# Kernel tuning notes

Hardware: AMD Instinct MI355X
Metric: run time of the kernel (lower is better)

## Reference

```python
import jax, jax.numpy as jnp
import numpy as np

LR = 0.01
DECAY = 0.9


def setup_inputs() -> dict:
    key = jax.random.key(0)
    ks = jax.random.split(key, 8)
    B, D_IN, H, N_FLUX, N_MET, N_IN, N_REF = 32768, 128, 1024, 512, 256, 128, 64
    return {
        "input": jax.random.normal(ks[0], (B, D_IN), jnp.float32),
        "Vref": jax.random.normal(ks[1], (B, N_REF), jnp.float32),
        "Vin": jax.random.normal(ks[2], (B, N_IN), jnp.float32),
        "W1": jax.random.normal(ks[3], (D_IN, H), jnp.float32) * 0.02,
        "b1": jnp.zeros((H,), jnp.float32),
        "W2": jax.random.normal(ks[4], (H, N_FLUX), jnp.float32) * 0.02,
        "b2": jnp.zeros((N_FLUX,), jnp.float32),
        "S": jax.random.normal(ks[5], (N_MET, N_FLUX), jnp.float32) * 0.1,
        "Pin": jax.random.normal(ks[6], (N_IN, N_FLUX), jnp.float32) * 0.1,
        "n_iteration": 30,
    }


def reference(input, Vref, Vin, W1, b1, W2, b2, S, Pin, n_iteration):
    # MLP head: Linear -> ReLU -> (Dropout inactive at eval) -> Linear
    V0 = jnp.maximum(input @ W1 + b1, 0.0) @ W2 + b2  # [B, n_flux]
    n_met = S.shape[0]
    n_in = Pin.shape[0]
    n_flux = V0.shape[1]

    def step(carry, _):
        V, diff = carry
        # dL2/dV = 2/n_met * (V S^T) S
        dV2 = (V @ S.T) @ S * (2.0 / n_met)
        # dL3/dV = 2/n_in * relu(V Pin^T - Vin) Pin  (indicator*relu == relu)
        relu_vin = jnp.maximum(V @ Pin.T - Vin, 0.0)
        dV3 = relu_vin @ Pin * (2.0 / n_in)
        # dL4/dV = -2/n_flux * relu(-V) = 2/n_flux * min(V, 0)
        dV4 = jnp.minimum(V, 0.0) * (2.0 / n_flux)
        dV = dV2 + dV3 + dV4
        diff_new = DECAY * diff - LR * dV
        return (V + diff_new, diff_new), None

    (V, _), _ = jax.lax.scan(step, (V0, jnp.zeros_like(V0)), None, length=n_iteration)
    return V
```

## Files before the change

### kernel.cpp

```cpp
#include <hip/hip_runtime.h>

typedef __bf16 bhalf;
typedef __bf16 bh8_t __attribute__((ext_vector_type(8)));
typedef float f4_t __attribute__((ext_vector_type(4)));

#define MFMA16(A, B, C) __builtin_amdgcn_mfma_f32_16x16x32_bf16((A), (B), (C), 0, 0, 0)


#define OFF_W1T  0
#define OFF_W2T  (OFF_W1T + 1024 * 128)
#define OFF_PINB (OFF_W2T + 512 * 1024)
#define OFF_PT   (OFF_PINB + 128 * 512)
#define OFF_G    (OFF_PT + 512 * 128)

__global__ __launch_bounds__(256) void amn_prep(
    const float* __restrict__ W1, const float* __restrict__ W2,
    const float* __restrict__ Pin, bhalf* __restrict__ ws) {
  unsigned i = blockIdx.x * 256u + threadIdx.x;
  if (i < 131072u) {
    unsigned n = i >> 7, k = i & 127u;
    ws[OFF_W1T + i] = (bhalf)W1[k * 1024u + n];
  } else if (i < 655360u) {
    unsigned j = i - 131072u;
    unsigned n = j >> 10, k = j & 1023u;
    ws[OFF_W2T + j] = (bhalf)W2[k * 512u + n];
  } else if (i < 720896u) {
    unsigned j = i - 655360u;
    ws[OFF_PINB + j] = (bhalf)Pin[j];
  } else if (i < 786432u) {
    unsigned j = i - 720896u;
    unsigned n = j >> 7, k = j & 127u;
    ws[OFF_PT + j] = (bhalf)(Pin[k * 512u + n] * 0.015625f);
  }
}

__global__ __launch_bounds__(256) void amn_gram(
    const float* __restrict__ S, bhalf* __restrict__ ws) {
  const unsigned bi = blockIdx.x >> 5, bj = blockIdx.x & 31u;
  __shared__ float SA[256][16];
  __shared__ float SB[256][16];
  const unsigned t = threadIdx.x;
#pragma unroll
  for (int p = 0; p < 16; ++p) {
    unsigned e = p * 256u + t;
    unsigned k = e >> 4, c = e & 15u;
    SA[k][c] = S[k * 512u + bi * 16u + c];
    SB[k][c] = S[k * 512u + bj * 16u + c];
  }
  __syncthreads();
  const unsigned ti = t >> 4, tj = t & 15u;
  float acc = 0.f;
#pragma unroll 8
  for (int k = 0; k < 256; ++k) acc += SA[k][ti] * SB[k][tj];
  ws[OFF_G + (bi * 16u + ti) * 512u + bj * 16u + tj] = (bhalf)(acc * 0.0078125f);
}

__device__ inline bh8_t cvt8(f4_t f0, f4_t f1) {
  bh8_t r;
  r[0] = (bhalf)f0[0]; r[1] = (bhalf)f0[1]; r[2] = (bhalf)f0[2]; r[3] = (bhalf)f0[3];
  r[4] = (bhalf)f1[0]; r[5] = (bhalf)f1[1]; r[6] = (bhalf)f1[2]; r[7] = (bhalf)f1[3];
  return r;
}
__device__ inline unsigned pk2(float a, float b) {
  union { bhalf h; unsigned short s; } x, y;
  x.h = (bhalf)a; y.h = (bhalf)b;
  return (unsigned)x.s | ((unsigned)y.s << 16);
}
__device__ inline float up_lo(unsigned u) {
  union { unsigned u; float f; } t; t.u = u << 16; return t.f;
}
__device__ inline float up_hi(unsigned u) {
  union { unsigned u; float f; } t; t.u = u & 0xffff0000u; return t.f;
}

__device__ inline void gload16(const void* g, void* l) {
  __builtin_amdgcn_global_load_lds(
      (const __attribute__((address_space(1))) void*)g,
      (__attribute__((address_space(3))) void*)l, 16, 0, 0);
}

#define SMV   0
#define SMR   33280
#define SMB0  41984
#define BUFSTEP 40960
#define GSZ   32768
#define SMEM_BYTES 123904

__global__ __launch_bounds__(512) void amn_main(
    const float* __restrict__ input, const float* __restrict__ Vin,
    const float* __restrict__ b1, const float* __restrict__ b2,
    const int* __restrict__ niter_p,
    const bhalf* __restrict__ ws, float* __restrict__ out) {

  const unsigned tid = threadIdx.x;
  const unsigned w  = tid >> 6;
  const unsigned l  = tid & 63u;
  const unsigned lq = l >> 4;
  const unsigned lr = l & 15u;
  const unsigned row0 = blockIdx.x * 32u;
  const unsigned rq = l >> 2;
  const unsigned c16 = (l & 3u) * 16u;

  const bhalf* W1t  = ws + OFF_W1T;
  const bhalf* W2t  = ws + OFF_W2T;

  __shared__ __align__(16) unsigned char smem[SMEM_BYTES];
  bhalf* hid_lds = (bhalf*)smem;
  bhalf* V_lds   = (bhalf*)(smem + SMV);
  bhalf* R_lds   = (bhalf*)(smem + SMR);

  {
    f4_t hacc[2][8];
#pragma unroll
    for (int mt = 0; mt < 2; ++mt)
#pragma unroll
      for (int t = 0; t < 8; ++t) hacc[mt][t] = (f4_t)0.f;

#pragma unroll
    for (int k = 0; k < 4; ++k) {
      bh8_t a[2];
#pragma unroll
      for (int mt = 0; mt < 2; ++mt) {
        const float* ap = input + (row0 + 16u * mt + lr) * 128u + k * 32 + lq * 8u;
        a[mt] = cvt8(*(const f4_t*)ap, *(const f4_t*)(ap + 4));
      }
#pragma unroll
      for (int t = 0; t < 8; ++t) {
        bh8_t b = *(const bh8_t*)(W1t + (16u * (8u * w + t) + lr) * 128u + k * 32 + lq * 8u);
#pragma unroll
        for (int mt = 0; mt < 2; ++mt) hacc[mt][t] = MFMA16(a[mt], b, hacc[mt][t]);
      }
    }
#pragma unroll
    for (int t = 0; t < 8; ++t) {
      unsigned col = 16u * (8u * w + t) + lr;
      float bias = b1[col];
#pragma unroll
      for (int mt = 0; mt < 2; ++mt)
#pragma unroll
        for (int r = 0; r < 4; ++r)
          hid_lds[(16u * mt + 4u * lq + r) * 1032u + col] =
              (bhalf)fmaxf(hacc[mt][t][r] + bias, 0.f);
    }
  }
  __syncthreads();

  f4_t Vreg[2][4];
#pragma unroll
  for (int mt = 0; mt < 2; ++mt)
#pragma unroll
    for (int n = 0; n < 4; ++n) Vreg[mt][n] = (f4_t)0.f;

#pragma unroll 2
  for (int k = 0; k < 32; ++k) {
    bh8_t a[2];
#pragma unroll
    for (int mt = 0; mt < 2; ++mt)
      a[mt] = *(const bh8_t*)(hid_lds + (16u * mt + lr) * 1032u + k * 32 + lq * 8u);
#pragma unroll
    for (int n = 0; n < 4; ++n) {
      bh8_t b = *(const bh8_t*)(W2t + (16u * (4u * w + n) + lr) * 1024u + k * 32 + lq * 8u);
#pragma unroll
      for (int mt = 0; mt < 2; ++mt) Vreg[mt][n] = MFMA16(a[mt], b, Vreg[mt][n]);
    }
  }
#pragma unroll
  for (int n = 0; n < 4; ++n) {
    float bias = b2[16u * (4u * w + n) + lr];
#pragma unroll
    for (int mt = 0; mt < 2; ++mt)
#pragma unroll
      for (int r = 0; r < 4; ++r) Vreg[mt][n][r] += bias;
  }

  unsigned Vinpk[2][2];
#pragma unroll
  for (int mt = 0; mt < 2; ++mt) {
    float vi[4];
#pragma unroll
    for (int r = 0; r < 4; ++r)
      vi[r] = Vin[(row0 + 16u * mt + 4u * lq + r) * 128u + 16u * w + lr];
    Vinpk[mt][0] = pk2(vi[0], vi[1]);
    Vinpk[mt][1] = pk2(vi[2], vi[3]);
  }

  unsigned Dpk[2][4][2];
#pragma unroll
  for (int mt = 0; mt < 2; ++mt)
#pragma unroll
    for (int n = 0; n < 4; ++n) { Dpk[mt][n][0] = 0u; Dpk[mt][n][1] = 0u; }

  const int niter = niter_p[0];

  asm volatile("s_waitcnt vmcnt(0)" ::: "memory");
  __syncthreads();

  const char* Gb  = (const char*)(ws + OFF_G);
  const char* Pb  = (const char*)(ws + OFF_PINB);
  const char* Ptb = (const char*)(ws + OFF_PT);

  for (int it = 0; it < niter; ++it) {
#pragma unroll
    for (int mt = 0; mt < 2; ++mt)
#pragma unroll
      for (int n = 0; n < 4; ++n) {
        unsigned col = 16u * (4u * w + n) + lr;
#pragma unroll
        for (int r = 0; r < 4; ++r)
          V_lds[(16u * mt + 4u * lq + r) * 520u + col] = (bhalf)Vreg[mt][n][r];
      }
    __syncthreads();

    f4_t dacc[4][2];
#pragma unroll
    for (int nt = 0; nt < 4; ++nt) { dacc[nt][0] = (f4_t)0.f; dacc[nt][1] = (f4_t)0.f; }
    f4_t Uacc[2];
    Uacc[0] = (f4_t)0.f; Uacc[1] = (f4_t)0.f;

    {
      unsigned b = SMB0;
#pragma unroll
      for (int i = 0; i < 4; ++i) {
        unsigned s = w + 8u * i;
        gload16(Gb + ((16u * s + rq) * 512u) * 2u + c16, smem + b + s * 1024u);
      }
      gload16(Pb + ((16u * w + rq) * 512u) * 2u + c16, smem + b + GSZ + w * 1024u);
    }

#pragma unroll 1
    for (int t = 0; t < 16; ++t) {
      asm volatile("s_waitcnt lgkmcnt(0)" ::: "memory");
      __builtin_amdgcn_s_barrier();
      __builtin_amdgcn_sched_barrier(0);
      if (t < 15) {
        unsigned u = (unsigned)t + 1u;
        unsigned b = SMB0 + (u & 1u) * BUFSTEP;
#pragma unroll
        for (int i = 0; i < 4; ++i) {
          unsigned s = w + 8u * i;
          gload16(Gb + ((16u * s + rq) * 512u + u * 32u) * 2u + c16, smem + b + s * 1024u);
        }
        gload16(Pb + ((16u * w + rq) * 512u + u * 32u) * 2u + c16, smem + b + GSZ + w * 1024u);
        asm volatile("s_waitcnt vmcnt(5)" ::: "memory");
      } else {
        unsigned b = SMB0;
#pragma unroll
        for (int i = 0; i < 4; ++i) {
          unsigned s = w + 8u * i;
          gload16(Ptb + ((16u * s + rq) * 128u) * 2u + c16, smem + b + s * 1024u);
        }
        asm volatile("s_waitcnt vmcnt(4)" ::: "memory");
      }
      __builtin_amdgcn_s_barrier();
      __builtin_amdgcn_sched_barrier(0);

      const bhalf* gb = (const bhalf*)(smem + SMB0 + ((unsigned)t & 1u) * BUFSTEP);
      const bhalf* pb = gb + GSZ / 2;
      bh8_t a0 = *(const bh8_t*)(V_lds + lr * 520u + t * 32 + lq * 8u);
      bh8_t a1 = *(const bh8_t*)(V_lds + (16u + lr) * 520u + t * 32 + lq * 8u);
#pragma unroll
      for (int nt = 0; nt < 4; ++nt) {
        bh8_t bfr = *(const bh8_t*)(gb + (16u * (4u * w + nt) + lr) * 32u + lq * 8u);
        dacc[nt][0] = MFMA16(a0, bfr, dacc[nt][0]);
        dacc[nt][1] = MFMA16(a1, bfr, dacc[nt][1]);
      }
      bh8_t pf = *(const bh8_t*)(pb + (16u * w + lr) * 32u + lq * 8u);
      Uacc[0] = MFMA16(a0, pf, Uacc[0]);
      Uacc[1] = MFMA16(a1, pf, Uacc[1]);
    }

#pragma unroll
    for (int mt = 0; mt < 2; ++mt) {
      float v0 = up_lo(Vinpk[mt][0]), v1 = up_hi(Vinpk[mt][0]);
      float v2 = up_lo(Vinpk[mt][1]), v3 = up_hi(Vinpk[mt][1]);
      unsigned base = (16u * mt + 4u * lq) * 136u + 16u * w + lr;
      R_lds[base]        = (bhalf)fmaxf(Uacc[mt][0] - v0, 0.f);
      R_lds[base + 136u] = (bhalf)fmaxf(Uacc[mt][1] - v1, 0.f);
      R_lds[base + 272u] = (bhalf)fmaxf(Uacc[mt][2] - v2, 0.f);
      R_lds[base + 408u] = (bhalf)fmaxf(Uacc[mt][3] - v3, 0.f);
    }

#pragma unroll 1
    for (int t2 = 0; t2 < 4; ++t2) {
      asm volatile("s_waitcnt lgkmcnt(0)" ::: "memory");
      __builtin_amdgcn_s_barrier();
      __builtin_amdgcn_sched_barrier(0);
      if (t2 < 3) {
        unsigned kc2 = (unsigned)t2 + 1u;
        unsigned b = SMB0 + (kc2 & 1u) * BUFSTEP;
#pragma unroll
        for (int i = 0; i < 4; ++i) {
          unsigned s = w + 8u * i;
          gload16(Ptb + ((16u * s + rq) * 128u + kc2 * 32u) * 2u + c16, smem + b + s * 1024u);
        }
        asm volatile("s_waitcnt vmcnt(4)" ::: "memory");
      } else {
        asm volatile("s_waitcnt vmcnt(0)" ::: "memory");
      }
      __builtin_amdgcn_s_barrier();
      __builtin_amdgcn_sched_barrier(0);

      const bhalf* gb = (const bhalf*)(smem + SMB0 + ((unsigned)t2 & 1u) * BUFSTEP);
      bh8_t a0 = *(const bh8_t*)(R_lds + lr * 136u + t2 * 32 + lq * 8u);
      bh8_t a1 = *(const bh8_t*)(R_lds + (16u + lr) * 136u + t2 * 32 + lq * 8u);
#pragma unroll
      for (int nt = 0; nt < 4; ++nt) {
        bh8_t bfr = *(const bh8_t*)(gb + (16u * (4u * w + nt) + lr) * 32u + lq * 8u);
        dacc[nt][0] = MFMA16(a0, bfr, dacc[nt][0]);
        dacc[nt][1] = MFMA16(a1, bfr, dacc[nt][1]);
      }
    }

#pragma unroll
    for (int nt = 0; nt < 4; ++nt)
#pragma unroll
      for (int mt = 0; mt < 2; ++mt) {
        float dv0 = dacc[nt][mt][0] + fminf(Vreg[mt][nt][0], 0.f) * 0.00390625f;
        float dv1 = dacc[nt][mt][1] + fminf(Vreg[mt][nt][1], 0.f) * 0.00390625f;
        float dv2 = dacc[nt][mt][2] + fminf(Vreg[mt][nt][2], 0.f) * 0.00390625f;
        float dv3 = dacc[nt][mt][3] + fminf(Vreg[mt][nt][3], 0.f) * 0.00390625f;
        float d0 = 0.9f * up_lo(Dpk[mt][nt][0]) - 0.01f * dv0;
        float d1 = 0.9f * up_hi(Dpk[mt][nt][0]) - 0.01f * dv1;
        float d2 = 0.9f * up_lo(Dpk[mt][nt][1]) - 0.01f * dv2;
        float d3 = 0.9f * up_hi(Dpk[mt][nt][1]) - 0.01f * dv3;
        Vreg[mt][nt][0] += d0; Vreg[mt][nt][1] += d1;
        Vreg[mt][nt][2] += d2; Vreg[mt][nt][3] += d3;
        Dpk[mt][nt][0] = pk2(d0, d1);
        Dpk[mt][nt][1] = pk2(d2, d3);
      }
  }

#pragma unroll
  for (int mt = 0; mt < 2; ++mt)
#pragma unroll
    for (int n = 0; n < 4; ++n) {
      unsigned col = 16u * (4u * w + n) + lr;
#pragma unroll
      for (int r = 0; r < 4; ++r)
        out[(row0 + 16u * mt + 4u * lq + r) * 512u + col] = Vreg[mt][n][r];
    }
}

extern "C" void kernel_launch(void* const* d_in, const int* in_sizes, int n_in,
                              void* d_out, int out_size, void* d_ws, size_t ws_size,
                              hipStream_t stream) {
  const float* input = (const float*)d_in[0];
  const float* Vin = (const float*)d_in[2];
  const float* W1  = (const float*)d_in[3];
  const float* b1  = (const float*)d_in[4];
  const float* W2  = (const float*)d_in[5];
  const float* b2  = (const float*)d_in[6];
  const float* S   = (const float*)d_in[7];
  const float* Pin = (const float*)d_in[8];
  const int* nit   = (const int*)d_in[9];
  bhalf* ws  = (bhalf*)d_ws;
  float* out = (float*)d_out;

  amn_prep<<<3072, 256, 0, stream>>>(W1, W2, Pin, ws);
  amn_gram<<<1024, 256, 0, stream>>>(S, ws);
  amn_main<<<1024, 512, 0, stream>>>(input, Vin, b1, b2, nit, ws, out);
}
```

Baseline: 1.721 ms.

## Single-buffer G/P tiles with XOR-swizzled V and R LDS layout

Replaces the double-buffered weight-tile staging in LDS with a single buffer, shrinking shared memory from about 121 KB to 80 KB. The padded V and R layouts become XOR-swizzled 16-byte chunk layouts meant to avoid bank conflicts. The relu(Vin) residual is now written during the last G-tile step. The smaller LDS footprint could allow two 512-thread blocks per CU. In exchange, global-to-LDS loads are no longer overlapped with MFMA compute: each step waits on vmcnt(0) between compute phases.

```diff
diff --git a/kernel.cpp b/kernel.cpp
--- a/kernel.cpp
+++ b/kernel.cpp
@@ -72,6 +72,7 @@
 __device__ inline float up_hi(unsigned u) {
   union { unsigned u; float f; } t; t.u = u & 0xffff0000u; return t.f;
 }
+__device__ inline unsigned rot3(unsigned r) { return ((r & 1u) << 2) | ((r >> 1) & 3u); }
 
 __device__ inline void gload16(const void* g, void* l) {
   __builtin_amdgcn_global_load_lds(
@@ -80,11 +81,10 @@
 }
 
 #define SMV   0
-#define SMR   33280
-#define SMB0  41984
-#define BUFSTEP 40960
-#define GSZ   32768
-#define SMEM_BYTES 123904
+#define SMR   32768
+#define SMB   40960
+#define SMP   73728
+#define SMEM_BYTES 81920
 
 __global__ __launch_bounds__(512) void amn_main(
     const float* __restrict__ input, const float* __restrict__ Vin,
@@ -98,16 +98,14 @@
   const unsigned lq = l >> 4;
   const unsigned lr = l & 15u;
   const unsigned row0 = blockIdx.x * 32u;
-  const unsigned rq = l >> 2;
+  const unsigned rq  = l >> 2;
   const unsigned c16 = (l & 3u) * 16u;
 
-  const bhalf* W1t  = ws + OFF_W1T;
-  const bhalf* W2t  = ws + OFF_W2T;
+  const bhalf* W1t = ws + OFF_W1T;
+  const bhalf* W2t = ws + OFF_W2T;
 
   __shared__ __align__(16) unsigned char smem[SMEM_BYTES];
   bhalf* hid_lds = (bhalf*)smem;
-  bhalf* V_lds   = (bhalf*)(smem + SMV);
-  bhalf* R_lds   = (bhalf*)(smem + SMR);
 
   {
     f4_t hacc[2][8];
@@ -204,12 +202,26 @@
     for (int mt = 0; mt < 2; ++mt)
 #pragma unroll
       for (int n = 0; n < 4; ++n) {
-        unsigned col = 16u * (4u * w + n) + lr;
-#pragma unroll
-        for (int r = 0; r < 4; ++r)
-          V_lds[(16u * mt + 4u * lq + r) * 520u + col] = (bhalf)Vreg[mt][n][r];
-      }
-    __syncthreads();
+        unsigned chunk0 = 2u * (4u * w + n) + (lr >> 3);
+        unsigned wi = (lr & 7u) * 2u;
+#pragma unroll
+        for (int r = 0; r < 4; ++r) {
+          unsigned row = 16u * mt + 4u * lq + r;
+          *(bhalf*)(smem + SMV + row * 1024u +
+                    ((chunk0 ^ rot3(row & 7u)) << 4) + wi) = (bhalf)Vreg[mt][n][r];
+        }
+      }
+    asm volatile("s_waitcnt lgkmcnt(0)" ::: "memory");
+
+#pragma unroll
+    for (int i = 0; i < 4; ++i) {
+      unsigned s = w + 8u * i;
+      gload16(Gb + ((16u * s + rq) * 512u) * 2u + c16, smem + SMB + s * 1024u);
+    }
+    gload16(Pb + ((16u * w + rq) * 512u) * 2u + c16, smem + SMP + w * 1024u);
+    asm volatile("s_waitcnt vmcnt(0)" ::: "memory");
+    __builtin_amdgcn_s_barrier();
+    __builtin_amdgcn_sched_barrier(0);
 
     f4_t dacc[4][2];
 #pragma unroll
@@ -217,97 +229,91 @@
     f4_t Uacc[2];
     Uacc[0] = (f4_t)0.f; Uacc[1] = (f4_t)0.f;
 
-    {
-      unsigned b = SMB0;
-#pragma unroll
-      for (int i = 0; i < 4; ++i) {
-        unsigned s = w + 8u * i;
-        gload16(Gb + ((16u * s + rq) * 512u) * 2u + c16, smem + b + s * 1024u);
-      }
-      gload16(Pb + ((16u * w + rq) * 512u) * 2u + c16, smem + b + GSZ + w * 1024u);
-    }
-
 #pragma unroll 1
     for (int t = 0; t < 16; ++t) {
+      {
+        unsigned vph = (((unsigned)(4 * t) + lq) ^ rot3(lr & 7u)) << 4;
+        bh8_t a0 = *(const bh8_t*)(smem + SMV + lr * 1024u + vph);
+        bh8_t a1 = *(const bh8_t*)(smem + SMV + (16u + lr) * 1024u + vph);
+        const bhalf* gb = (const bhalf*)(smem + SMB);
+        const bhalf* pb = (const bhalf*)(smem + SMP);
+#pragma unroll
+        for (int nt = 0; nt < 4; ++nt) {
+          bh8_t bfr = *(const bh8_t*)(gb + (16u * (4u * w + nt) + lr) * 32u + lq * 8u);
+          dacc[nt][0] = MFMA16(a0, bfr, dacc[nt][0]);
+          dacc[nt][1] = MFMA16(a1, bfr, dacc[nt][1]);
+        }
+        bh8_t pf = *(const bh8_t*)(pb + (16u * w + lr) * 32u + lq * 8u);
+        Uacc[0] = MFMA16(a0, pf, Uacc[0]);
+        Uacc[1] = MFMA16(a1, pf, Uacc[1]);
+      }
       asm volatile("s_waitcnt lgkmcnt(0)" ::: "memory");
       __builtin_amdgcn_s_barrier();
       __builtin_amdgcn_sched_barrier(0);
+
       if (t < 15) {
         unsigned u = (unsigned)t + 1u;
-        unsigned b = SMB0 + (u & 1u) * BUFSTEP;
 #pragma unroll
         for (int i = 0; i < 4; ++i) {
           unsigned s = w + 8u * i;
-          gload16(Gb + ((16u * s + rq) * 512u + u * 32u) * 2u + c16, smem + b + s * 1024u);
-        }
-        gload16(Pb + ((16u * w + rq) * 512u + u * 32u) * 2u + c16, smem + b + GSZ + w * 1024u);
-        asm volatile("s_waitcnt vmcnt(5)" ::: "memory");
+          gload16(Gb + ((16u * s + rq) * 512u + u * 32u) * 2u + c16, smem + SMB + s * 1024u);
+        }
+        gload16(Pb + ((16u * w + rq) * 512u + u * 32u) * 2u + c16, smem + SMP + w * 1024u);
+        asm volatile("s_waitcnt vmcnt(0)" ::: "memory");
       } else {
-        unsigned b = SMB0;
 #pragma unroll
         for (int i = 0; i < 4; ++i) {
           unsigned s = w + 8u * i;
-          gload16(Ptb + ((16u * s + rq) * 128u) * 2u + c16, smem + b + s * 1024u);
-        }
-        asm volatile("s_waitcnt vmcnt(4)" ::: "memory");
+          gload16(Ptb + ((16u * s + rq) * 128u) * 2u + c16, smem + SMB + s * 1024u);
+        }
+#pragma unroll
+        for (int mt = 0; mt < 2; ++mt) {
+          float v0 = up_lo(Vinpk[mt][0]), v1 = up_hi(Vinpk[mt][0]);
+          float v2 = up_lo(Vinpk[mt][1]), v3 = up_hi(Vinpk[mt][1]);
+          float rv[4] = { fmaxf(Uacc[mt][0] - v0, 0.f), fmaxf(Uacc[mt][1] - v1, 0.f),
+                          fmaxf(Uacc[mt][2] - v2, 0.f), fmaxf(Uacc[mt][3] - v3, 0.f) };
+          unsigned chunk0 = 2u * w + (lr >> 3);
+          unsigned wi = (lr & 7u) * 2u;
+#pragma unroll
+          for (int r = 0; r < 4; ++r) {
+            unsigned row = 16u * mt + 4u * lq + r;
+            *(bhalf*)(smem + SMR + row * 256u +
+                      ((chunk0 ^ rot3(row & 7u)) << 4) + wi) = (bhalf)rv[r];
+          }
+        }
+        asm volatile("s_waitcnt vmcnt(0) lgkmcnt(0)" ::: "memory");
       }
       __builtin_amdgcn_s_barrier();
       __builtin_amdgcn_sched_barrier(0);
-
-      const bhalf* gb = (const bhalf*)(smem + SMB0 + ((unsigned)t & 1u) * BUFSTEP);
-      const bhalf* pb = gb + GSZ / 2;
-      bh8_t a0 = *(const bh8_t*)(V_lds + lr * 520u + t * 32 + lq * 8u);
-      bh8_t a1 = *(const bh8_t*)(V_lds + (16u + lr) * 520u + t * 32 + lq * 8u);
-#pragma unroll
-      for (int nt = 0; nt < 4; ++nt) {
-        bh8_t bfr = *(const bh8_t*)(gb + (16u * (4u * w + nt) + lr) * 32u + lq * 8u);
-        dacc[nt][0] = MFMA16(a0, bfr, dacc[nt][0]);
-        dacc[nt][1] = MFMA16(a1, bfr, dacc[nt][1]);
-      }
-      bh8_t pf = *(const bh8_t*)(pb + (16u * w + lr) * 32u + lq * 8u);
-      Uacc[0] = MFMA16(a0, pf, Uacc[0]);
-      Uacc[1] = MFMA16(a1, pf, Uacc[1]);
-    }
-
-#pragma unroll
-    for (int mt = 0; mt < 2; ++mt) {
-      float v0 = up_lo(Vinpk[mt][0]), v1 = up_hi(Vinpk[mt][0]);
-      float v2 = up_lo(Vinpk[mt][1]), v3 = up_hi(Vinpk[mt][1]);
-      unsigned base = (16u * mt + 4u * lq) * 136u + 16u * w + lr;
-      R_lds[base]        = (bhalf)fmaxf(Uacc[mt][0] - v0, 0.f);
-      R_lds[base + 136u] = (bhalf)fmaxf(Uacc[mt][1] - v1, 0.f);
-      R_lds[base + 272u] = (bhalf)fmaxf(Uacc[mt][2] - v2, 0.f);
-      R_lds[base + 408u] = (bhalf)fmaxf(Uacc[mt][3] - v3, 0.f);
     }
 
 #pragma unroll 1
     for (int t2 = 0; t2 < 4; ++t2) {
+      {
+        unsigned rph = (((unsigned)(4 * t2) + lq) ^ rot3(lr & 7u)) << 4;
+        bh8_t a0 = *(const bh8_t*)(smem + SMR + lr * 256u + rph);
+        bh8_t a1 = *(const bh8_t*)(smem + SMR + (16u + lr) * 256u + rph);
+        const bhalf* gb = (const bhalf*)(smem + SMB);
+#pragma unroll
+        for (int nt = 0; nt < 4; ++nt) {
+          bh8_t bfr = *(const bh8_t*)(gb + (16u * (4u * w + nt) + lr) * 32u + lq * 8u);
+          dacc[nt][0] = MFMA16(a0, bfr, dacc[nt][0]);
+          dacc[nt][1] = MFMA16(a1, bfr, dacc[nt][1]);
+        }
+      }
       asm volatile("s_waitcnt lgkmcnt(0)" ::: "memory");
       __builtin_amdgcn_s_barrier();
       __builtin_amdgcn_sched_barrier(0);
       if (t2 < 3) {
-        unsigned kc2 = (unsigned)t2 + 1u;
-        unsigned b = SMB0 + (kc2 & 1u) * BUFSTEP;
+        unsigned kc = (unsigned)t2 + 1u;
 #pragma unroll
         for (int i = 0; i < 4; ++i) {
           unsigned s = w + 8u * i;
-          gload16(Ptb + ((16u * s + rq) * 128u + kc2 * 32u) * 2u + c16, smem + b + s * 1024u);
-        }
-        asm volatile("s_waitcnt vmcnt(4)" ::: "memory");
-      } else {
+          gload16(Ptb + ((16u * s + rq) * 128u + kc * 32u) * 2u + c16, smem + SMB + s * 1024u);
+        }
         asm volatile("s_waitcnt vmcnt(0)" ::: "memory");
-      }
-      __builtin_amdgcn_s_barrier();
-      __builtin_amdgcn_sched_barrier(0);
-
-      const bhalf* gb = (const bhalf*)(smem + SMB0 + ((unsigned)t2 & 1u) * BUFSTEP);
-      bh8_t a0 = *(const bh8_t*)(R_lds + lr * 136u + t2 * 32 + lq * 8u);
-      bh8_t a1 = *(const bh8_t*)(R_lds + (16u + lr) * 136u + t2 * 32 + lq * 8u);
-#pragma unroll
-      for (int nt = 0; nt < 4; ++nt) {
-        bh8_t bfr = *(const bh8_t*)(gb + (16u * (4u * w + nt) + lr) * 32u + lq * 8u);
-        dacc[nt][0] = MFMA16(a0, bfr, dacc[nt][0]);
-        dacc[nt][1] = MFMA16(a1, bfr, dacc[nt][1]);
+        __builtin_amdgcn_s_barrier();
+        __builtin_amdgcn_sched_barrier(0);
       }
     }
 
```

After: 2.307 ms. 34.0% more time.

## Triple-buffer G/Pin/Pt tile loads with one barrier per k-step

Applied to the files above, without the earlier changes.

Replaces the double-buffered LDS staging of the G, Pin and Pt tiles with a three-buffer ring. Loads are issued two steps ahead, and each k-step now uses a single barrier instead of two. The R tile is stored in an XOR-like rotated layout with row stride 128 instead of padding, and per-thread global offsets are precomputed. The goal is to hide global-to-LDS latency and cut barrier stalls, at the cost of more LDS per block, which could reduce occupancy.

```diff
diff --git a/kernel.cpp b/kernel.cpp
--- a/kernel.cpp
+++ b/kernel.cpp
@@ -79,12 +79,62 @@
       (__attribute__((address_space(3))) void*)l, 16, 0, 0);
 }
 
-#define SMV   0
-#define SMR   33280
-#define SMB0  41984
-#define BUFSTEP 40960
-#define GSZ   32768
-#define SMEM_BYTES 123904
+#define SMBUF 33280u
+#define BUFSZ 40960u
+#define PREG  32768u
+#define RBASE 147968u
+#define SMEM_BYTES 156160
+
+#define LGKM0   asm volatile("s_waitcnt lgkmcnt(0)" ::: "memory")
+#define VMW(N)  asm volatile("s_waitcnt vmcnt(" #N ")" ::: "memory")
+#define SCHEDB  __builtin_amdgcn_sched_barrier(0)
+#define RAWBAR  __builtin_amdgcn_s_barrier()
+
+#define ISSUE_GP(BO, KC) do {                                                   \
+  _Pragma("unroll")                                                             \
+  for (int i_ = 0; i_ < 4; ++i_) {                                              \
+    unsigned s_ = w + 8u * i_;                                                  \
+    gload16(Gb + gsb[i_] + (KC) * 64u, smem + SMBUF + (BO) + s_ * 1024u);       \
+  }                                                                             \
+  gload16(Pb + psb + (KC) * 64u, smem + SMBUF + (BO) + PREG + w * 1024u);       \
+} while (0)
+
+#define ISSUE_PT(BO, KC) do {                                                   \
+  _Pragma("unroll")                                                             \
+  for (int i_ = 0; i_ < 4; ++i_) {                                              \
+    unsigned s_ = w + 8u * i_;                                                  \
+    gload16(Ptb + ptsb[i_] + (KC) * 64u, smem + SMBUF + (BO) + s_ * 1024u);     \
+  }                                                                             \
+} while (0)
+
+#define COMPUTE_GP(BO, T) do {                                                  \
+  const bhalf* gb_ = (const bhalf*)(smem + SMBUF + (BO));                       \
+  const bhalf* pb_ = gb_ + 16384u;                                              \
+  bh8_t a0_ = *(const bh8_t*)(V_lds + lr * 520u + (T) * 32u + lq * 8u);         \
+  bh8_t a1_ = *(const bh8_t*)(V_lds + (16u + lr) * 520u + (T) * 32u + lq * 8u); \
+  _Pragma("unroll")                                                             \
+  for (int nt_ = 0; nt_ < 4; ++nt_) {                                           \
+    bh8_t bf_ = *(const bh8_t*)(gb_ + (16u * (4u * w + nt_) + lr) * 32u + lq * 8u);\
+    dacc[nt_][0] = MFMA16(a0_, bf_, dacc[nt_][0]);                              \
+    dacc[nt_][1] = MFMA16(a1_, bf_, dacc[nt_][1]);                              \
+  }                                                                             \
+  bh8_t pf_ = *(const bh8_t*)(pb_ + (16u * w + lr) * 32u + lq * 8u);            \
+  Uacc[0] = MFMA16(a0_, pf_, Uacc[0]);                                          \
+  Uacc[1] = MFMA16(a1_, pf_, Uacc[1]);                                          \
+} while (0)
+
+#define COMPUTE_PT(BO, C) do {                                                  \
+  const bhalf* gb_ = (const bhalf*)(smem + SMBUF + (BO));                       \
+  unsigned ro0_ = ((C) * 32u + lq * 8u + 8u * lr) & 127u;                       \
+  bh8_t a0_ = *(const bh8_t*)(R_lds + lr * 128u + ro0_);                        \
+  bh8_t a1_ = *(const bh8_t*)(R_lds + (16u + lr) * 128u + ro0_);                \
+  _Pragma("unroll")                                                             \
+  for (int nt_ = 0; nt_ < 4; ++nt_) {                                           \
+    bh8_t bf_ = *(const bh8_t*)(gb_ + (16u * (4u * w + nt_) + lr) * 32u + lq * 8u);\
+    dacc[nt_][0] = MFMA16(a0_, bf_, dacc[nt_][0]);                              \
+    dacc[nt_][1] = MFMA16(a1_, bf_, dacc[nt_][1]);                              \
+  }                                                                             \
+} while (0)
 
 __global__ __launch_bounds__(512) void amn_main(
     const float* __restrict__ input, const float* __restrict__ Vin,
@@ -98,16 +148,19 @@
   const unsigned lq = l >> 4;
   const unsigned lr = l & 15u;
   const unsigned row0 = blockIdx.x * 32u;
-  const unsigned rq = l >> 2;
+  const unsigned rq  = l >> 2;
   const unsigned c16 = (l & 3u) * 16u;
 
-  const bhalf* W1t  = ws + OFF_W1T;
-  const bhalf* W2t  = ws + OFF_W2T;
+  const bhalf* W1t = ws + OFF_W1T;
+  const bhalf* W2t = ws + OFF_W2T;
+  const char* Gb  = (const char*)(ws + OFF_G);
+  const char* Pb  = (const char*)(ws + OFF_PINB);
+  const char* Ptb = (const char*)(ws + OFF_PT);
 
   __shared__ __align__(16) unsigned char smem[SMEM_BYTES];
   bhalf* hid_lds = (bhalf*)smem;
-  bhalf* V_lds   = (bhalf*)(smem + SMV);
-  bhalf* R_lds   = (bhalf*)(smem + SMR);
+  bhalf* V_lds   = (bhalf*)smem;
+  bhalf* R_lds   = (bhalf*)(smem + RBASE);
 
   {
     f4_t hacc[2][8];
@@ -190,15 +243,20 @@
 #pragma unroll
     for (int n = 0; n < 4; ++n) { Dpk[mt][n][0] = 0u; Dpk[mt][n][1] = 0u; }
 
+  unsigned gsb[4], ptsb[4];
+#pragma unroll
+  for (int j = 0; j < 4; ++j) {
+    unsigned s = w + 8u * j;
+    gsb[j]  = (16u * s + rq) * 1024u + c16;
+    ptsb[j] = (16u * s + rq) * 256u + c16;
+  }
+  const unsigned psb = (16u * w + rq) * 1024u + c16;
+
   const int niter = niter_p[0];
 
   asm volatile("s_waitcnt vmcnt(0)" ::: "memory");
   __syncthreads();
 
-  const char* Gb  = (const char*)(ws + OFF_G);
-  const char* Pb  = (const char*)(ws + OFF_PINB);
-  const char* Ptb = (const char*)(ws + OFF_PT);
-
   for (int it = 0; it < niter; ++it) {
 #pragma unroll
     for (int mt = 0; mt < 2; ++mt)
@@ -209,7 +267,10 @@
         for (int r = 0; r < 4; ++r)
           V_lds[(16u * mt + 4u * lq + r) * 520u + col] = (bhalf)Vreg[mt][n][r];
       }
-    __syncthreads();
+    LGKM0; SCHEDB; RAWBAR; SCHEDB;
+
+    ISSUE_GP(0u, 0u);
+    ISSUE_GP(BUFSZ, 1u);
 
     f4_t dacc[4][2];
 #pragma unroll
@@ -217,99 +278,49 @@
     f4_t Uacc[2];
     Uacc[0] = (f4_t)0.f; Uacc[1] = (f4_t)0.f;
 
-    {
-      unsigned b = SMB0;
-#pragma unroll
-      for (int i = 0; i < 4; ++i) {
-        unsigned s = w + 8u * i;
-        gload16(Gb + ((16u * s + rq) * 512u) * 2u + c16, smem + b + s * 1024u);
-      }
-      gload16(Pb + ((16u * w + rq) * 512u) * 2u + c16, smem + b + GSZ + w * 1024u);
-    }
-
+    unsigned cur = 0u;
 #pragma unroll 1
-    for (int t = 0; t < 16; ++t) {
-      asm volatile("s_waitcnt lgkmcnt(0)" ::: "memory");
-      __builtin_amdgcn_s_barrier();
-      __builtin_amdgcn_sched_barrier(0);
-      if (t < 15) {
-        unsigned u = (unsigned)t + 1u;
-        unsigned b = SMB0 + (u & 1u) * BUFSTEP;
-#pragma unroll
-        for (int i = 0; i < 4; ++i) {
-          unsigned s = w + 8u * i;
-          gload16(Gb + ((16u * s + rq) * 512u + u * 32u) * 2u + c16, smem + b + s * 1024u);
-        }
-        gload16(Pb + ((16u * w + rq) * 512u + u * 32u) * 2u + c16, smem + b + GSZ + w * 1024u);
-        asm volatile("s_waitcnt vmcnt(5)" ::: "memory");
-      } else {
-        unsigned b = SMB0;
-#pragma unroll
-        for (int i = 0; i < 4; ++i) {
-          unsigned s = w + 8u * i;
-          gload16(Ptb + ((16u * s + rq) * 128u) * 2u + c16, smem + b + s * 1024u);
-        }
-        asm volatile("s_waitcnt vmcnt(4)" ::: "memory");
-      }
-      __builtin_amdgcn_s_barrier();
-      __builtin_amdgcn_sched_barrier(0);
-
-      const bhalf* gb = (const bhalf*)(smem + SMB0 + ((unsigned)t & 1u) * BUFSTEP);
-      const bhalf* pb = gb + GSZ / 2;
-      bh8_t a0 = *(const bh8_t*)(V_lds + lr * 520u + t * 32 + lq * 8u);
-      bh8_t a1 = *(const bh8_t*)(V_lds + (16u + lr) * 520u + t * 32 + lq * 8u);
-#pragma unroll
-      for (int nt = 0; nt < 4; ++nt) {
-        bh8_t bfr = *(const bh8_t*)(gb + (16u * (4u * w + nt) + lr) * 32u + lq * 8u);
-        dacc[nt][0] = MFMA16(a0, bfr, dacc[nt][0]);
-        dacc[nt][1] = MFMA16(a1, bfr, dacc[nt][1]);
-      }
-      bh8_t pf = *(const bh8_t*)(pb + (16u * w + lr) * 32u + lq * 8u);
-      Uacc[0] = MFMA16(a0, pf, Uacc[0]);
-      Uacc[1] = MFMA16(a1, pf, Uacc[1]);
-    }
-
+    for (int t = 0; t < 14; ++t) {
+      VMW(5); SCHEDB; RAWBAR; SCHEDB;
+      COMPUTE_GP(cur, (unsigned)t);
+      LGKM0; SCHEDB;
+      unsigned o2 = cur + 2u * BUFSZ; if (o2 >= 3u * BUFSZ) o2 -= 3u * BUFSZ;
+      ISSUE_GP(o2, (unsigned)t + 2u);
+      cur += BUFSZ; if (cur >= 3u * BUFSZ) cur = 0u;
+    }
+    VMW(5); SCHEDB; RAWBAR; SCHEDB;
+    COMPUTE_GP(2u * BUFSZ, 14u);
+    LGKM0; SCHEDB;
+    ISSUE_PT(BUFSZ, 0u);
+    VMW(4); SCHEDB; RAWBAR; SCHEDB;
+    COMPUTE_GP(0u, 15u);
 #pragma unroll
     for (int mt = 0; mt < 2; ++mt) {
-      float v0 = up_lo(Vinpk[mt][0]), v1 = up_hi(Vinpk[mt][0]);
-      float v2 = up_lo(Vinpk[mt][1]), v3 = up_hi(Vinpk[mt][1]);
-      unsigned base = (16u * mt + 4u * lq) * 136u + 16u * w + lr;
-      R_lds[base]        = (bhalf)fmaxf(Uacc[mt][0] - v0, 0.f);
-      R_lds[base + 136u] = (bhalf)fmaxf(Uacc[mt][1] - v1, 0.f);
-      R_lds[base + 272u] = (bhalf)fmaxf(Uacc[mt][2] - v2, 0.f);
-      R_lds[base + 408u] = (bhalf)fmaxf(Uacc[mt][3] - v3, 0.f);
-    }
-
-#pragma unroll 1
-    for (int t2 = 0; t2 < 4; ++t2) {
-      asm volatile("s_waitcnt lgkmcnt(0)" ::: "memory");
-      __builtin_amdgcn_s_barrier();
-      __builtin_amdgcn_sched_barrier(0);
-      if (t2 < 3) {
-        unsigned kc2 = (unsigned)t2 + 1u;
-        unsigned b = SMB0 + (kc2 & 1u) * BUFSTEP;
-#pragma unroll
-        for (int i = 0; i < 4; ++i) {
-          unsigned s = w + 8u * i;
-          gload16(Ptb + ((16u * s + rq) * 128u + kc2 * 32u) * 2u + c16, smem + b + s * 1024u);
-        }
-        asm volatile("s_waitcnt vmcnt(4)" ::: "memory");
-      } else {
-        asm volatile("s_waitcnt vmcnt(0)" ::: "memory");
-      }
-      __builtin_amdgcn_s_barrier();
-      __builtin_amdgcn_sched_barrier(0);
-
-      const bhalf* gb = (const bhalf*)(smem + SMB0 + ((unsigned)t2 & 1u) * BUFSTEP);
-      bh8_t a0 = *(const bh8_t*)(R_lds + lr * 136u + t2 * 32 + lq * 8u);
-      bh8_t a1 = *(const bh8_t*)(R_lds + (16u + lr) * 136u + t2 * 32 + lq * 8u);
-#pragma unroll
-      for (int nt = 0; nt < 4; ++nt) {
-        bh8_t bfr = *(const bh8_t*)(gb + (16u * (4u * w + nt) + lr) * 32u + lq * 8u);
-        dacc[nt][0] = MFMA16(a0, bfr, dacc[nt][0]);
-        dacc[nt][1] = MFMA16(a1, bfr, dacc[nt][1]);
-      }
-    }
+      float rv[4] = { fmaxf(Uacc[mt][0] - up_lo(Vinpk[mt][0]), 0.f),
+                      fmaxf(Uacc[mt][1] - up_hi(Vinpk[mt][0]), 0.f),
+                      fmaxf(Uacc[mt][2] - up_lo(Vinpk[mt][1]), 0.f),
+                      fmaxf(Uacc[mt][3] - up_hi(Vinpk[mt][1]), 0.f) };
+      unsigned col = 16u * w + lr;
+#pragma unroll
+      for (int r = 0; r < 4; ++r) {
+        unsigned row = 16u * mt + 4u * lq + r;
+        R_lds[row * 128u + ((col + 8u * row) & 127u)] = (bhalf)rv[r];
+      }
+    }
+    LGKM0; SCHEDB;
+    ISSUE_PT(2u * BUFSZ, 1u);
+    VMW(4); SCHEDB; RAWBAR; SCHEDB;
+    COMPUTE_PT(BUFSZ, 0u);
+    LGKM0; SCHEDB;
+    ISSUE_PT(0u, 2u);
+    VMW(4); SCHEDB; RAWBAR; SCHEDB;
+    COMPUTE_PT(2u * BUFSZ, 1u);
+    LGKM0; SCHEDB;
+    ISSUE_PT(BUFSZ, 3u);
+    VMW(4); SCHEDB; RAWBAR; SCHEDB;
+    COMPUTE_PT(0u, 2u);
+    VMW(0); SCHEDB; RAWBAR; SCHEDB;
+    COMPUTE_PT(BUFSZ, 3u);
 
 #pragma unroll
     for (int nt = 0; nt < 4; ++nt)
```

New measurement: 1.695 ms. No clear change (-1.5%).
